# Optimization experiments

Measured on AMD Instinct MI355X. Metric: run time of the kernel, lower is better.

The kernel has to match this reference:

```python
import jax, jax.numpy as jnp
import numpy as np

DIM, CDIM, CSIZE = 512, 128, 8192
EPS = 1e-6


def setup_inputs() -> dict:
    key = jax.random.key(0)
    k = jax.random.split(key, 5)
    x = jax.random.normal(k[0], (4, 4096, DIM), jnp.float32)
    codebook = jax.random.normal(k[1], (CSIZE, CDIM), jnp.float32) * CDIM ** -0.5
    W1 = jax.random.normal(k[2], (CDIM, DIM), jnp.float32) * CDIM ** -0.5
    b1 = jnp.zeros((DIM,), jnp.float32)
    W2 = jax.random.normal(k[3], (DIM, DIM), jnp.float32) * DIM ** -0.5
    b2 = jnp.zeros((DIM,), jnp.float32)
    return dict(x=x, codebook=codebook, W1=W1, b1=b1, W2=W2, b2=b2)


def _code_transform(cb, W1, b1, W2, b2):
    # linear then residual(SELU -> linear):  h + Linear(SELU(h))
    h = cb @ W1 + b1                      # [C, dim]
    return h + jax.nn.selu(h) @ W2 + b2


def _rotate_to(src, tgt):
    # Householder-based rotation trick; only src (=x) carries gradient.
    ns = jnp.linalg.norm(src, axis=-1, keepdims=True)
    nt = jnp.linalg.norm(tgt, axis=-1, keepdims=True)
    u = jax.lax.stop_gradient(src / jnp.maximum(ns, EPS))
    q = jax.lax.stop_gradient(tgt / jnp.maximum(nt, EPS))
    w = u + q
    w = jax.lax.stop_gradient(w / jnp.maximum(jnp.linalg.norm(w, axis=-1, keepdims=True), EPS))
    rot = (src
           - 2.0 * jnp.sum(src * w, -1, keepdims=True) * w
           + 2.0 * jnp.sum(src * u, -1, keepdims=True) * q)
    return rot * jax.lax.stop_gradient(nt / jnp.maximum(ns, EPS))


def reference(x, codebook, W1, b1, W2, b2):
    # implicit codebook through learned transform  [C, dim]
    icb = _code_transform(codebook, W1, b1, W2, b2)
    # nearest-code search (no_grad in original): squared euclidean, argmin
    x_sg = jax.lax.stop_gradient(x)
    icb_sg = jax.lax.stop_gradient(icb)
    d2 = (jnp.sum(x_sg * x_sg, -1, keepdims=True)
          - 2.0 * jnp.einsum('bnd,cd->bnc', x_sg, icb_sg)
          + jnp.sum(icb_sg * icb_sg, -1))          # [B,N,C]
    indices = jnp.argmin(d2, axis=-1)               # [B,N]
    quantized = icb[indices]                        # [B,N,dim]
    commit_loss = (jnp.mean((jax.lax.stop_gradient(x) - quantized) ** 2)
                   + 0.25 * jnp.mean((x - jax.lax.stop_gradient(quantized)) ** 2))
    quantized = _rotate_to(x, quantized)
    return quantized, indices, commit_loss
```

## Files before the change

kernel.cpp:

```cpp
#include <hip/hip_runtime.h>
#include <math.h>

#define DIM   512
#define CDIM  128
#define CSIZE 8192
#define NTOK  16384
#define EPSV  1e-6f
#define NSLICE 16

#define SELU_SCALE 1.0507009873554805f
#define SELU_ALPHA 1.6732632423543772f

typedef __bf16 bf16x8 __attribute__((ext_vector_type(8)));
typedef float  f32x4  __attribute__((ext_vector_type(4)));
typedef unsigned short u16x8 __attribute__((ext_vector_type(8)));

__device__ __forceinline__ float selu_f(float v) {
    return SELU_SCALE * (v > 0.f ? v : SELU_ALPHA * expm1f(v));
}

__device__ __forceinline__ unsigned short b16(float f) {
    unsigned u = __float_as_uint(f);
    u += 0x7FFFu + ((u >> 16) & 1u);
    return (unsigned short)(u >> 16);
}
__device__ __forceinline__ float b2f(unsigned short h) {
    return __uint_as_float(((unsigned)h) << 16);
}

__device__ __forceinline__ unsigned SWZ(unsigned b) {
    return b ^ (((b >> 6) & 14u) << 3);
}

#define GLOAD16(g, l) __builtin_amdgcn_global_load_lds( \
    (const __attribute__((address_space(1))) void*)(g),  \
    (__attribute__((address_space(3))) void*)(l), 16, 0, 0)

__global__ __launch_bounds__(256) void k_init(float* __restrict__ rn2,
                                              float* __restrict__ lossacc) {
    const int i = blockIdx.x * 256 + threadIdx.x;
    if (i < CSIZE) rn2[i] = 0.f;
    if (i < 64)    lossacc[i] = 0.f;
}

__global__ void k_fin(const float* __restrict__ lossacc, float* __restrict__ out_loss) {
    float v = lossacc[threadIdx.x];
#pragma unroll
    for (int o = 1; o < 64; o <<= 1) v += __shfl_xor(v, o);
    if (threadIdx.x == 0)
        out_loss[0] = 1.25f * v / (float)((size_t)NTOK * DIM);
}

__global__ __launch_bounds__(256) void k_split(const float* __restrict__ in,
                                               unsigned short* __restrict__ hi,
                                               unsigned short* __restrict__ lo,
                                               int n4) {
    const int i = blockIdx.x * 256 + threadIdx.x;
    if (i >= n4) return;
    const float4 v = ((const float4*)in)[i];
    const unsigned short h0 = b16(v.x), h1 = b16(v.y), h2 = b16(v.z), h3 = b16(v.w);
    const unsigned short l0 = b16(v.x - b2f(h0));
    const unsigned short l1 = b16(v.y - b2f(h1));
    const unsigned short l2 = b16(v.z - b2f(h2));
    const unsigned short l3 = b16(v.w - b2f(h3));
    ((ushort4*)hi)[i] = make_ushort4(h0, h1, h2, h3);
    ((ushort4*)lo)[i] = make_ushort4(l0, l1, l2, l3);
}

__global__ __launch_bounds__(256) void k_splitT(const float* __restrict__ W,
                                                unsigned short* __restrict__ Thi,
                                                unsigned short* __restrict__ Tlo,
                                                int K, int N) {
    __shared__ float t[32][33];
    const int tx = threadIdx.x & 31, ty = threadIdx.x >> 5;
    const int n0 = blockIdx.x * 32, k0 = blockIdx.y * 32;
#pragma unroll
    for (int i = 0; i < 4; ++i)
        t[ty + i * 8][tx] = W[(size_t)(k0 + ty + i * 8) * N + n0 + tx];
    __syncthreads();
#pragma unroll
    for (int i = 0; i < 4; ++i) {
        const int n = n0 + ty + i * 8, k = k0 + tx;
        const float v = t[tx][ty + i * 8];
        const unsigned short h = b16(v);
        Thi[(size_t)n * K + k] = h;
        Tlo[(size_t)n * K + k] = b16(v - b2f(h));
    }
}

template<int KTOT, bool OUT_SPLIT>
__global__ __launch_bounds__(256) void k_gemm(const float* __restrict__ A,
                                              const unsigned short* __restrict__ BThi,
                                              const unsigned short* __restrict__ BTlo,
                                              const float* __restrict__ bias,
                                              const float* __restrict__ res,
                                              float* __restrict__ outF,
                                              unsigned short* __restrict__ outHi,
                                              unsigned short* __restrict__ outLo,
                                              float* __restrict__ rn2) {
    __shared__ __align__(16) unsigned char smem[24576];
    const int tid = threadIdx.x;
    const int wave = tid >> 6, lane = tid & 63;
    const int l15 = lane & 15, l4 = lane >> 4;
    const int m0 = blockIdx.x * 128, n0 = blockIdx.y * 64;
    const int wm0 = (wave >> 1) * 64, wn0 = (wave & 1) * 32;

    const unsigned LB = SWZ((unsigned)tid * 16u);
    const int soffB = (int)(LB >> 6) * KTOT + (int)((LB >> 4) & 3) * 8;

    const unsigned ra0 = SWZ((unsigned)((wm0 + l15) * 64 + l4 * 16));
    const unsigned rb0 = SWZ((unsigned)((wn0 + l15) * 64 + l4 * 16));

    f32x4 acc[4][2];
#pragma unroll
    for (int a = 0; a < 4; ++a)
#pragma unroll
        for (int b = 0; b < 2; ++b) acc[a][b] = (f32x4)(0.f);

    for (int k0 = 0; k0 < KTOT; k0 += 32) {
        __syncthreads();
        GLOAD16(BThi + (size_t)n0 * KTOT + k0 + soffB, smem + 16384 + wave * 1024);
        GLOAD16(BTlo + (size_t)n0 * KTOT + k0 + soffB, smem + 20480 + wave * 1024);
#pragma unroll
        for (int r = 0; r < 2; ++r) {
            const unsigned g = (unsigned)(tid + r * 256) * 16u;
            const int grow = (int)(g >> 6), gel = (int)((g >> 4) & 3) * 8;
            const float4 v0 = *(const float4*)(A + (size_t)(m0 + grow) * KTOT + k0 + gel);
            const float4 v1 = *(const float4*)(A + (size_t)(m0 + grow) * KTOT + k0 + gel + 4);
            float s[8] = {v0.x, v0.y, v0.z, v0.w, v1.x, v1.y, v1.z, v1.w};
            u16x8 hv, lv;
#pragma unroll
            for (int j = 0; j < 8; ++j) {
                const float sv = OUT_SPLIT ? selu_f(s[j]) : s[j];
                const unsigned short hb = b16(sv);
                hv[j] = hb;
                lv[j] = b16(sv - b2f(hb));
            }
            const unsigned d = SWZ(g);
            *(u16x8*)(smem + d) = hv;
            *(u16x8*)(smem + 8192 + d) = lv;
        }
        __syncthreads();

        bf16x8 bh[2], bl[2];
#pragma unroll
        for (int ni = 0; ni < 2; ++ni) {
            bh[ni] = *(const bf16x8*)(smem + 16384 + rb0 + ni * 1024);
            bl[ni] = *(const bf16x8*)(smem + 20480 + rb0 + ni * 1024);
        }
#pragma unroll
        for (int mi = 0; mi < 4; ++mi) {
            const bf16x8 ah = *(const bf16x8*)(smem + ra0 + mi * 1024);
            const bf16x8 al = *(const bf16x8*)(smem + 8192 + ra0 + mi * 1024);
#pragma unroll
            for (int ni = 0; ni < 2; ++ni) {
                acc[mi][ni] = __builtin_amdgcn_mfma_f32_16x16x32_bf16(ah, bh[ni], acc[mi][ni], 0, 0, 0);
                acc[mi][ni] = __builtin_amdgcn_mfma_f32_16x16x32_bf16(ah, bl[ni], acc[mi][ni], 0, 0, 0);
                acc[mi][ni] = __builtin_amdgcn_mfma_f32_16x16x32_bf16(al, bh[ni], acc[mi][ni], 0, 0, 0);
            }
        }
    }
#pragma unroll
    for (int mi = 0; mi < 4; ++mi)
#pragma unroll
        for (int rr = 0; rr < 4; ++rr) {
            const int m = m0 + wm0 + mi * 16 + l4 * 4 + rr;
            float s2 = 0.f;
#pragma unroll
            for (int ni = 0; ni < 2; ++ni) {
                const int n = n0 + wn0 + ni * 16 + l15;
                float v = acc[mi][ni][rr] + bias[n];
                if constexpr (OUT_SPLIT) {
                    v += res[(size_t)m * DIM + n];
                    const unsigned short hb = b16(v);
                    outHi[(size_t)m * DIM + n] = hb;
                    outLo[(size_t)m * DIM + n] = b16(v - b2f(hb));
                    s2 = fmaf(v, v, s2);
                } else {
                    outF[(size_t)m * DIM + n] = v;
                }
            }
            if constexpr (OUT_SPLIT) {
#pragma unroll
                for (int o = 1; o < 16; o <<= 1) s2 += __shfl_xor(s2, o);
                if (l15 == 0) atomicAdd(&rn2[m], s2);
            }
        }
}

__global__ __launch_bounds__(256, 2) void k_dist(const unsigned short* __restrict__ xh,
                                                 const unsigned short* __restrict__ xl,
                                                 const unsigned short* __restrict__ ch,
                                                 const unsigned short* __restrict__ cl,
                                                 const float* __restrict__ rn2,
                                                 float* __restrict__ pval,
                                                 int*   __restrict__ pidx) {
    __shared__ __align__(16) unsigned char smem[49152];
    const int tid  = threadIdx.x;
    const int wave = tid >> 6, lane = tid & 63;
    const int l15 = lane & 15, l4 = lane >> 4;
    const int m0   = blockIdx.x * 256;
    const int wm0  = (wave >> 1) * 128;
    const int wn0  = (wave & 1) * 64;

    const unsigned LS = SWZ((unsigned)tid * 16u);
    const int soff0 = (int)(LS >> 6) * DIM + (int)((LS >> 4) & 3) * 8;

    const unsigned ra0 = SWZ((unsigned)((wm0 + l15) * 64 + l4 * 16));
    const unsigned rb0 = SWZ((unsigned)((wn0 + l15) * 64 + l4 * 16));

    float bestv[8][4];
    int   besti[8][4];
#pragma unroll
    for (int a = 0; a < 8; ++a)
#pragma unroll
        for (int b = 0; b < 4; ++b) { bestv[a][b] = 3.0e38f; besti[a][b] = 0; }

    const unsigned short* xhb = xh + (size_t)m0 * DIM;
    const unsigned short* xlb = xl + (size_t)m0 * DIM;
    const int cbase = blockIdx.y * (CSIZE / NSLICE);

    for (int nt = 0; nt < (CSIZE / NSLICE) / 128; ++nt) {
        const int n0 = cbase + nt * 128;
        const unsigned short* chb = ch + (size_t)n0 * DIM;
        const unsigned short* clb = cl + (size_t)n0 * DIM;

        f32x4 acc[8][4];
#pragma unroll
        for (int a = 0; a < 8; ++a)
#pragma unroll
            for (int b = 0; b < 4; ++b) acc[a][b] = (f32x4)(0.f);

        for (int k0 = 0; k0 < DIM; k0 += 32) {
            __syncthreads();
            const int sA = soff0 + k0;
#pragma unroll
            for (int r = 0; r < 4; ++r) {
                GLOAD16(xhb + sA + r * 64 * DIM, smem + 0     + r * 4096 + wave * 1024);
                GLOAD16(xlb + sA + r * 64 * DIM, smem + 16384 + r * 4096 + wave * 1024);
            }
#pragma unroll
            for (int r = 0; r < 2; ++r) {
                GLOAD16(chb + sA + r * 64 * DIM, smem + 32768 + r * 4096 + wave * 1024);
                GLOAD16(clb + sA + r * 64 * DIM, smem + 40960 + r * 4096 + wave * 1024);
            }
            __syncthreads();

            bf16x8 bh[4], bl[4];
#pragma unroll
            for (int ni = 0; ni < 4; ++ni) {
                bh[ni] = *(const bf16x8*)(smem + 32768 + rb0 + ni * 1024);
                bl[ni] = *(const bf16x8*)(smem + 40960 + rb0 + ni * 1024);
            }
#pragma unroll
            for (int mi = 0; mi < 8; ++mi) {
                const bf16x8 ah = *(const bf16x8*)(smem + ra0 + mi * 1024);
                const bf16x8 al = *(const bf16x8*)(smem + 16384 + ra0 + mi * 1024);
#pragma unroll
                for (int ni = 0; ni < 4; ++ni) {
                    acc[mi][ni] = __builtin_amdgcn_mfma_f32_16x16x32_bf16(ah, bh[ni], acc[mi][ni], 0, 0, 0);
                    acc[mi][ni] = __builtin_amdgcn_mfma_f32_16x16x32_bf16(ah, bl[ni], acc[mi][ni], 0, 0, 0);
                    acc[mi][ni] = __builtin_amdgcn_mfma_f32_16x16x32_bf16(al, bh[ni], acc[mi][ni], 0, 0, 0);
                }
            }
        }

#pragma unroll
        for (int ni = 0; ni < 4; ++ni) {
            const int n = n0 + wn0 + ni * 16 + l15;
            const float r = rn2[n];
#pragma unroll
            for (int mi = 0; mi < 8; ++mi)
#pragma unroll
                for (int rr = 0; rr < 4; ++rr) {
                    const float v = fmaf(-2.f, acc[mi][ni][rr], r);
                    if (v < bestv[mi][rr]) { bestv[mi][rr] = v; besti[mi][rr] = n; }
                }
        }
    }

    __syncthreads();
    float* vbuf = (float*)smem;
    int*   ibuf = (int*)(smem + 2048);
#pragma unroll
    for (int mi = 0; mi < 8; ++mi)
#pragma unroll
        for (int rr = 0; rr < 4; ++rr) {
            float v = bestv[mi][rr];
            int   id = besti[mi][rr];
#pragma unroll
            for (int o = 1; o < 16; o <<= 1) {
                const float ov = __shfl_xor(v, o);
                const int   oid = __shfl_xor(id, o);
                if (ov < v || (ov == v && oid < id)) { v = ov; id = oid; }
            }
            if (l15 == 0) {
                const int ml = wm0 + mi * 16 + l4 * 4 + rr;
                vbuf[(wave & 1) * 256 + ml] = v;
                ibuf[(wave & 1) * 256 + ml] = id;
            }
        }
    __syncthreads();
    {
        const int ml = tid;
        float v0 = vbuf[ml], v1 = vbuf[256 + ml];
        int   i0 = ibuf[ml], i1 = ibuf[256 + ml];
        if (v1 < v0 || (v1 == v0 && i1 < i0)) { v0 = v1; i0 = i1; }
        pval[(size_t)blockIdx.y * NTOK + m0 + ml] = v0;
        pidx[(size_t)blockIdx.y * NTOK + m0 + ml] = i0;
    }
}

__global__ __launch_bounds__(256) void k_epi(const float* __restrict__ x,
                                             const unsigned short* __restrict__ chi,
                                             const unsigned short* __restrict__ clo,
                                             const float* __restrict__ pval,
                                             const int*   __restrict__ pidx,
                                             float* __restrict__ out_q,
                                             float* __restrict__ out_idx,
                                             float* __restrict__ lossacc) {
    const int wave = threadIdx.x >> 6, lane = threadIdx.x & 63;
    const int t = blockIdx.x * 4 + wave;

    float v = 3.0e38f; int id = 0;
    if (lane < NSLICE) {
        v  = pval[(size_t)lane * NTOK + t];
        id = pidx[(size_t)lane * NTOK + t];
    }
#pragma unroll
    for (int o = 1; o < 16; o <<= 1) {
        const float ov = __shfl_xor(v, o);
        const int   oid = __shfl_xor(id, o);
        if (ov < v || (ov == v && oid < id)) { v = ov; id = oid; }
    }
    id = __shfl(id, 0);

    const float4* xp = (const float4*)(x + (size_t)t * DIM);
    const float4 xv0 = xp[lane * 2];
    const float4 xv1 = xp[lane * 2 + 1];
    const u16x8 hv = *(const u16x8*)(chi + (size_t)id * DIM + lane * 8);
    const u16x8 lv = *(const u16x8*)(clo + (size_t)id * DIM + lane * 8);
    float q[8], xs[8] = {xv0.x, xv0.y, xv0.z, xv0.w, xv1.x, xv1.y, xv1.z, xv1.w};
#pragma unroll
    for (int j = 0; j < 8; ++j) q[j] = b2f(hv[j]) + b2f(lv[j]);

    float p0 = 0.f, p1 = 0.f, p2 = 0.f;
#pragma unroll
    for (int j = 0; j < 8; ++j) {
        p0 = fmaf(xs[j], xs[j], p0);
        p1 = fmaf(q[j], q[j], p1);
        p2 = fmaf(xs[j], q[j], p2);
    }
#pragma unroll
    for (int o = 1; o < 64; o <<= 1) {
        p0 += __shfl_xor(p0, o);
        p1 += __shfl_xor(p1, o);
        p2 += __shfl_xor(p2, o);
    }
    const float sx2 = p0, sq2 = p1, sxq = p2;

    const float ns  = sqrtf(sx2);
    const float nt  = sqrtf(sq2);
    const float nsc = fmaxf(ns, EPSV);
    const float ntc = fmaxf(nt, EPSV);
    const float xu  = sx2 / nsc;
    const float xqh = sxq / ntc;
    const float xw0 = xu + xqh;
    const float w0n2 = sx2 / (nsc * nsc) + 2.f * sxq / (nsc * ntc) + sq2 / (ntc * ntc);
    const float w0nc = fmaxf(sqrtf(w0n2), EPSV);
    const float coefW = 2.f * xw0 / (w0nc * w0nc);
    const float coefQ = 2.f * xu / ntc;
    const float scale = nt / nsc;
    const float cx = scale * (1.f - coefW / nsc);
    const float cq = scale * (coefQ - coefW / ntc);

    float4 ov0, ov1;
    ov0.x = cx * xs[0] + cq * q[0];  ov0.y = cx * xs[1] + cq * q[1];
    ov0.z = cx * xs[2] + cq * q[2];  ov0.w = cx * xs[3] + cq * q[3];
    ov1.x = cx * xs[4] + cq * q[4];  ov1.y = cx * xs[5] + cq * q[5];
    ov1.z = cx * xs[6] + cq * q[6];  ov1.w = cx * xs[7] + cq * q[7];
    ((float4*)(out_q + (size_t)t * DIM))[lane * 2]     = ov0;
    ((float4*)(out_q + (size_t)t * DIM))[lane * 2 + 1] = ov1;

    __shared__ float sew[4];
    if (lane == 0) {
        out_idx[t] = (float)id;
        sew[wave] = sx2 - 2.f * sxq + sq2;
    }
    __syncthreads();
    if (threadIdx.x == 0) {
        const float se = sew[0] + sew[1] + sew[2] + sew[3];
        atomicAdd(lossacc + (blockIdx.x & 63), se);
    }
}

extern "C" void kernel_launch(void* const* d_in, const int* in_sizes, int n_in,
                              void* d_out, int out_size, void* d_ws, size_t ws_size,
                              hipStream_t stream) {
    const float* x  = (const float*)d_in[0];
    const float* cb = (const float*)d_in[1];
    const float* W1 = (const float*)d_in[2];
    const float* b1 = (const float*)d_in[3];
    const float* W2 = (const float*)d_in[4];
    const float* b2 = (const float*)d_in[5];

    char* ws = (char*)d_ws;
    float* h = (float*)ws;
    unsigned short* chi = (unsigned short*)(h + (size_t)CSIZE * DIM);
    unsigned short* clo = chi + (size_t)CSIZE * DIM;
    unsigned short* W1Thi = clo + (size_t)CSIZE * DIM;
    unsigned short* W1Tlo = W1Thi + (size_t)DIM * CDIM;
    unsigned short* W2Thi = W1Tlo + (size_t)DIM * CDIM;
    unsigned short* W2Tlo = W2Thi + (size_t)DIM * DIM;
    float* rn2  = (float*)(W2Tlo + (size_t)DIM * DIM);
    float* pval = rn2 + CSIZE;
    int*   pidx = (int*)(pval + (size_t)NSLICE * NTOK);
    float* lossacc = (float*)(pidx + (size_t)NSLICE * NTOK);

    unsigned short* xhi = (unsigned short*)d_out;
    unsigned short* xlo = xhi + (size_t)NTOK * DIM;

    float* out_q    = (float*)d_out;
    float* out_idx  = out_q + (size_t)NTOK * DIM;
    float* out_loss = out_idx + NTOK;

    k_init<<<(CSIZE + 255) / 256, 256, 0, stream>>>(rn2, lossacc);
    k_split<<<(NTOK * DIM / 4) / 256, 256, 0, stream>>>(x, xhi, xlo, NTOK * DIM / 4);
    k_splitT<<<dim3(DIM / 32, CDIM / 32), 256, 0, stream>>>(W1, W1Thi, W1Tlo, CDIM, DIM);
    k_splitT<<<dim3(DIM / 32, DIM / 32), 256, 0, stream>>>(W2, W2Thi, W2Tlo, DIM, DIM);
    k_gemm<CDIM, false><<<dim3(CSIZE / 128, DIM / 64), 256, 0, stream>>>(
        cb, W1Thi, W1Tlo, b1, nullptr, h, nullptr, nullptr, nullptr);
    k_gemm<DIM, true><<<dim3(CSIZE / 128, DIM / 64), 256, 0, stream>>>(
        h, W2Thi, W2Tlo, b2, h, nullptr, chi, clo, rn2);
    k_dist<<<dim3(NTOK / 256, NSLICE), 256, 0, stream>>>(xhi, xlo, chi, clo, rn2, pval, pidx);
    k_epi<<<NTOK / 4, 256, 0, stream>>>(x, chi, clo, pval, pidx, out_q, out_idx, lossacc);
    k_fin<<<1, 64, 0, stream>>>(lossacc, out_loss);
}
```

Measured before the change: 530.4 us.

## Enlarge distance-kernel tile to 256x256 with 512 threads and double-buffered LDS

The distance GEMM block now covers 256 codes per tile instead of 128 and uses 8 waves. The codebook is split into 8 slices instead of 16, so each token tile is reloaded fewer times across slices. Global-to-LDS staging is double-buffered in a 128KB shared buffer, prefetching the next k-step while MFMAs run on the current one. The aim is to cut redundant x loads and hide load latency. The cost is far more LDS per block, which limits occupancy to about one block per CU, and fewer, larger blocks in the grid.

```diff
diff --git a/kernel.cpp b/kernel.cpp
--- a/kernel.cpp
+++ b/kernel.cpp
@@ -6,7 +6,7 @@
 #define CSIZE 8192
 #define NTOK  16384
 #define EPSV  1e-6f
-#define NSLICE 16
+#define NSLICE 8
 
 #define SELU_SCALE 1.0507009873554805f
 #define SELU_ALPHA 1.6732632423543772f
@@ -188,89 +188,99 @@
         }
 }
 
-__global__ __launch_bounds__(256, 2) void k_dist(const unsigned short* __restrict__ xh,
+__global__ __launch_bounds__(512, 2) void k_dist(const unsigned short* __restrict__ xh,
                                                  const unsigned short* __restrict__ xl,
                                                  const unsigned short* __restrict__ ch,
                                                  const unsigned short* __restrict__ cl,
                                                  const float* __restrict__ rn2,
                                                  float* __restrict__ pval,
                                                  int*   __restrict__ pidx) {
-    __shared__ __align__(16) unsigned char smem[49152];
+    __shared__ __align__(16) unsigned char smem[131072];
     const int tid  = threadIdx.x;
     const int wave = tid >> 6, lane = tid & 63;
     const int l15 = lane & 15, l4 = lane >> 4;
     const int m0   = blockIdx.x * 256;
-    const int wm0  = (wave >> 1) * 128;
-    const int wn0  = (wave & 1) * 64;
+    const int wm0  = (wave >> 1) * 64;
+    const int wn0  = (wave & 1) * 128;
 
     const unsigned LS = SWZ((unsigned)tid * 16u);
     const int soff0 = (int)(LS >> 6) * DIM + (int)((LS >> 4) & 3) * 8;
 
     const unsigned ra0 = SWZ((unsigned)((wm0 + l15) * 64 + l4 * 16));
     const unsigned rb0 = SWZ((unsigned)((wn0 + l15) * 64 + l4 * 16));
-
-    float bestv[8][4];
-    int   besti[8][4];
-#pragma unroll
-    for (int a = 0; a < 8; ++a)
-#pragma unroll
-        for (int b = 0; b < 4; ++b) { bestv[a][b] = 3.0e38f; besti[a][b] = 0; }
 
     const unsigned short* xhb = xh + (size_t)m0 * DIM;
     const unsigned short* xlb = xl + (size_t)m0 * DIM;
     const int cbase = blockIdx.y * (CSIZE / NSLICE);
 
-    for (int nt = 0; nt < (CSIZE / NSLICE) / 128; ++nt) {
-        const int n0 = cbase + nt * 128;
-        const unsigned short* chb = ch + (size_t)n0 * DIM;
-        const unsigned short* clb = cl + (size_t)n0 * DIM;
-
-        f32x4 acc[8][4];
-#pragma unroll
-        for (int a = 0; a < 8; ++a)
-#pragma unroll
-            for (int b = 0; b < 4; ++b) acc[a][b] = (f32x4)(0.f);
-
-        for (int k0 = 0; k0 < DIM; k0 += 32) {
+    constexpr int NT   = (CSIZE / NSLICE) / 256;
+    constexpr int TOTI = NT * (DIM / 32);
+
+    auto stage = [&](int iter, unsigned bufbase) {
+        const int nt2 = iter >> 4;
+        const int k0n = (iter & 15) * 32;
+        const int sA  = soff0 + k0n;
+        const size_t cb0 = (size_t)(cbase + nt2 * 256) * DIM;
+#pragma unroll
+        for (int r = 0; r < 2; ++r) {
+            GLOAD16(xhb + sA + r * 128 * DIM,      smem + bufbase + 0     + r * 8192 + wave * 1024);
+            GLOAD16(xlb + sA + r * 128 * DIM,      smem + bufbase + 16384 + r * 8192 + wave * 1024);
+            GLOAD16(ch + cb0 + sA + r * 128 * DIM, smem + bufbase + 32768 + r * 8192 + wave * 1024);
+            GLOAD16(cl + cb0 + sA + r * 128 * DIM, smem + bufbase + 49152 + r * 8192 + wave * 1024);
+        }
+    };
+
+    float bestv[4][4];
+    int   besti[4][4];
+#pragma unroll
+    for (int a = 0; a < 4; ++a)
+#pragma unroll
+        for (int b = 0; b < 4; ++b) { bestv[a][b] = 3.0e38f; besti[a][b] = 0; }
+
+    stage(0, 0u);
+    __syncthreads();
+    unsigned cur = 0;
+
+    for (int nt = 0; nt < NT; ++nt) {
+        f32x4 acc[4][8];
+#pragma unroll
+        for (int a = 0; a < 4; ++a)
+#pragma unroll
+            for (int b = 0; b < 8; ++b) acc[a][b] = (f32x4)(0.f);
+
+        for (int ks = 0; ks < 16; ++ks) {
+            const int iter = nt * 16 + ks;
+            if (iter + 1 < TOTI) stage(iter + 1, (cur ^ 1u) * 65536u);
+
+            const unsigned char* base = smem + cur * 65536u;
+            bf16x8 ah[4], al[4];
+#pragma unroll
+            for (int mi = 0; mi < 4; ++mi) {
+                ah[mi] = *(const bf16x8*)(base + ra0 + mi * 1024);
+                al[mi] = *(const bf16x8*)(base + 16384 + ra0 + mi * 1024);
+            }
+#pragma unroll
+            for (int ni = 0; ni < 8; ++ni) {
+                const bf16x8 bh = *(const bf16x8*)(base + 32768 + rb0 + ni * 1024);
+                const bf16x8 bl = *(const bf16x8*)(base + 49152 + rb0 + ni * 1024);
+#pragma unroll
+                for (int mi = 0; mi < 4; ++mi) {
+                    acc[mi][ni] = __builtin_amdgcn_mfma_f32_16x16x32_bf16(ah[mi], bh, acc[mi][ni], 0, 0, 0);
+                    acc[mi][ni] = __builtin_amdgcn_mfma_f32_16x16x32_bf16(ah[mi], bl, acc[mi][ni], 0, 0, 0);
+                    acc[mi][ni] = __builtin_amdgcn_mfma_f32_16x16x32_bf16(al[mi], bh, acc[mi][ni], 0, 0, 0);
+                }
+            }
             __syncthreads();
-            const int sA = soff0 + k0;
-#pragma unroll
-            for (int r = 0; r < 4; ++r) {
-                GLOAD16(xhb + sA + r * 64 * DIM, smem + 0     + r * 4096 + wave * 1024);
-                GLOAD16(xlb + sA + r * 64 * DIM, smem + 16384 + r * 4096 + wave * 1024);
-            }
-#pragma unroll
-            for (int r = 0; r < 2; ++r) {
-                GLOAD16(chb + sA + r * 64 * DIM, smem + 32768 + r * 4096 + wave * 1024);
-                GLOAD16(clb + sA + r * 64 * DIM, smem + 40960 + r * 4096 + wave * 1024);
-            }
-            __syncthreads();
-
-            bf16x8 bh[4], bl[4];
-#pragma unroll
-            for (int ni = 0; ni < 4; ++ni) {
-                bh[ni] = *(const bf16x8*)(smem + 32768 + rb0 + ni * 1024);
-                bl[ni] = *(const bf16x8*)(smem + 40960 + rb0 + ni * 1024);
-            }
-#pragma unroll
-            for (int mi = 0; mi < 8; ++mi) {
-                const bf16x8 ah = *(const bf16x8*)(smem + ra0 + mi * 1024);
-                const bf16x8 al = *(const bf16x8*)(smem + 16384 + ra0 + mi * 1024);
-#pragma unroll
-                for (int ni = 0; ni < 4; ++ni) {
-                    acc[mi][ni] = __builtin_amdgcn_mfma_f32_16x16x32_bf16(ah, bh[ni], acc[mi][ni], 0, 0, 0);
-                    acc[mi][ni] = __builtin_amdgcn_mfma_f32_16x16x32_bf16(ah, bl[ni], acc[mi][ni], 0, 0, 0);
-                    acc[mi][ni] = __builtin_amdgcn_mfma_f32_16x16x32_bf16(al, bh[ni], acc[mi][ni], 0, 0, 0);
-                }
-            }
-        }
-
-#pragma unroll
-        for (int ni = 0; ni < 4; ++ni) {
+            cur ^= 1u;
+        }
+
+        const int n0 = cbase + nt * 256;
+#pragma unroll
+        for (int ni = 0; ni < 8; ++ni) {
             const int n = n0 + wn0 + ni * 16 + l15;
             const float r = rn2[n];
 #pragma unroll
-            for (int mi = 0; mi < 8; ++mi)
+            for (int mi = 0; mi < 4; ++mi)
 #pragma unroll
                 for (int rr = 0; rr < 4; ++rr) {
                     const float v = fmaf(-2.f, acc[mi][ni][rr], r);
@@ -283,7 +293,7 @@
     float* vbuf = (float*)smem;
     int*   ibuf = (int*)(smem + 2048);
 #pragma unroll
-    for (int mi = 0; mi < 8; ++mi)
+    for (int mi = 0; mi < 4; ++mi)
 #pragma unroll
         for (int rr = 0; rr < 4; ++rr) {
             float v = bestv[mi][rr];
@@ -301,7 +311,7 @@
             }
         }
     __syncthreads();
-    {
+    if (tid < 256) {
         const int ml = tid;
         float v0 = vbuf[ml], v1 = vbuf[256 + ml];
         int   i0 = ibuf[ml], i1 = ibuf[256 + ml];
@@ -432,7 +442,7 @@
         cb, W1Thi, W1Tlo, b1, nullptr, h, nullptr, nullptr, nullptr);
     k_gemm<DIM, true><<<dim3(CSIZE / 128, DIM / 64), 256, 0, stream>>>(
         h, W2Thi, W2Tlo, b2, h, nullptr, chi, clo, rn2);
-    k_dist<<<dim3(NTOK / 256, NSLICE), 256, 0, stream>>>(xhi, xlo, chi, clo, rn2, pval, pidx);
+    k_dist<<<dim3(NTOK / 256, NSLICE), 512, 0, stream>>>(xhi, xlo, chi, clo, rn2, pval, pidx);
     k_epi<<<NTOK / 4, 256, 0, stream>>>(x, chi, clo, pval, pidx, out_q, out_idx, lossacc);
     k_fin<<<1, 64, 0, stream>>>(lossacc, out_loss);
 }
```

Result: faster. 485.5 us (-8.5%).
